# Kernel tuning notes

Measured on AMD Instinct MI355X. Metric: run time of the kernel, lower is better.

## Reference

```python
import jax, jax.numpy as jnp
import numpy as np

N_NODES = 100000
N_EDGES = 800000
IN_F = 128
HID = 128
OUT_F = 64


def setup_inputs() -> dict:
    key = jax.random.key(0)
    ks = jax.random.split(key, 13)
    s = 1.0 / np.sqrt(HID)
    return {
        "x": jax.random.normal(ks[0], (N_NODES, IN_F), jnp.float32),
        "src": jax.random.randint(ks[1], (N_EDGES,), 0, N_NODES, jnp.int32),
        "dst": jax.random.randint(ks[2], (N_EDGES,), 0, N_NODES, jnp.int32),
        "W1": jax.random.normal(ks[3], (HID, IN_F), jnp.float32) * s,
        "b1": jax.random.normal(ks[4], (HID,), jnp.float32) * s,
        "W2": jax.random.normal(ks[5], (HID, HID), jnp.float32) * s,
        "b2": jax.random.normal(ks[6], (HID,), jnp.float32) * s,
        "W3": jax.random.normal(ks[7], (HID, HID), jnp.float32) * s,
        "b3": jax.random.normal(ks[8], (HID,), jnp.float32) * s,
        "Wo1": jax.random.normal(ks[9], (HID, HID), jnp.float32) * s,
        "bo1": jax.random.normal(ks[10], (HID,), jnp.float32) * s,
        "Wo2": jax.random.normal(ks[11], (OUT_F, HID), jnp.float32) * s,
        "bo2": jax.random.normal(ks[12], (OUT_F,), jnp.float32) * s,
    }


def _mean_agg(h, src, dst, n_nodes):
    # mean over incoming edges (DGL copy_u -> mean reducer); isolated nodes get 0
    summed = jax.ops.segment_sum(h[src], dst, num_segments=n_nodes)
    deg = jax.ops.segment_sum(jnp.ones_like(src, h.dtype), dst, num_segments=n_nodes)
    return summed / jnp.maximum(deg, 1.0)[:, None]


def _lin(h, W, b):
    return h @ W.T + b


def reference(x, src, dst, W1, b1, W2, b2, W3, b3, Wo1, bo1, Wo2, bo2):
    n = x.shape[0]
    # x1 = fc1(x); x = relu(x1); x2 = fc2(x)
    x2 = _lin(jax.nn.relu(_lin(x, W1, b1)), W2, b2)
    # gin1: apply_func = Sequential(fc1, relu, fc2) on (x2 + mean_agg(x2)), eps=0
    h = x2 + _mean_agg(x2, src, dst, n)
    h = _lin(jax.nn.relu(_lin(h, W1, b1)), W2, b2)
    # x3 = fc3(h); h = relu(x3)
    h = jax.nn.relu(_lin(h, W3, b3))
    # gin2: apply_func = Sequential(fc3, relu) on (h + mean_agg(h))
    h = h + _mean_agg(h, src, dst, n)
    h = jax.nn.relu(_lin(h, W3, b3))
    # output head
    h = jax.nn.relu(_lin(h, Wo1, bo1))
    return _lin(h, Wo2, bo2)
```

## Files before the change

kernel.cpp:

```cpp
#include <hip/hip_runtime.h>

#define NNODES 100000
#define NEDGES 800000
#define NTILE128 782
#define NROWPAD (NTILE128*128)

typedef _Float16 f16x8 __attribute__((ext_vector_type(8)));
typedef float    f32x4 __attribute__((ext_vector_type(4)));
typedef unsigned int u32;
typedef unsigned short u16;

__global__ __launch_bounds__(256) void hist_kernel(const int* __restrict__ dst,
                                                   int* __restrict__ counts, int nE) {
    int i = blockIdx.x * 256 + threadIdx.x;
    if (i < nE) atomicAdd(counts + dst[i], 1);
}

__global__ __launch_bounds__(256) void scan1_kernel(const int* __restrict__ counts,
                                                    int* __restrict__ bsum, int n) {
    __shared__ int s[256];
    int i = blockIdx.x * 256 + threadIdx.x;
    s[threadIdx.x] = (i < n) ? counts[i] : 0;
    __syncthreads();
    for (int off = 128; off > 0; off >>= 1) {
        if (threadIdx.x < off) s[threadIdx.x] += s[threadIdx.x + off];
        __syncthreads();
    }
    if (threadIdx.x == 0) bsum[blockIdx.x] = s[0];
}

__global__ __launch_bounds__(512) void scan2_kernel(int* __restrict__ bsum, int nb) {
    __shared__ int s[512];
    int t = threadIdx.x;
    int orig = (t < nb) ? bsum[t] : 0;
    s[t] = orig;
    __syncthreads();
    for (int off = 1; off < 512; off <<= 1) {
        int v = (t >= off) ? s[t - off] : 0;
        __syncthreads();
        s[t] += v;
        __syncthreads();
    }
    if (t < nb) bsum[t] = s[t] - orig;
}

__global__ __launch_bounds__(256) void scan3_kernel(int* __restrict__ counts,
                                                    const int* __restrict__ boff,
                                                    int* __restrict__ rowptr, int n) {
    __shared__ int s[256];
    int i = blockIdx.x * 256 + threadIdx.x;
    int t = threadIdx.x;
    int orig = (i < n) ? counts[i] : 0;
    s[t] = orig;
    __syncthreads();
    for (int off = 1; off < 256; off <<= 1) {
        int v = (t >= off) ? s[t - off] : 0;
        __syncthreads();
        s[t] += v;
        __syncthreads();
    }
    if (i < n) {
        rowptr[i] = boff[blockIdx.x] + s[t] - orig;
        counts[i] = 0;
    }
    if (i == n - 1) rowptr[n] = boff[blockIdx.x] + s[t];
}

__global__ __launch_bounds__(256) void fill_kernel(const int* __restrict__ src,
                                                   const int* __restrict__ dst,
                                                   const int* __restrict__ rowptr,
                                                   int* __restrict__ cur,
                                                   int* __restrict__ eidx, int nE) {
    int i = blockIdx.x * 256 + threadIdx.x;
    if (i >= nE) return;
    int d = dst[i];
    int p = atomicAdd(cur + d, 1);
    eidx[rowptr[d] + p] = src[i];
}

__global__ __launch_bounds__(256) void gather_kernel(const _Float16* __restrict__ H,
                                                     const int* __restrict__ rowptr,
                                                     const int* __restrict__ eidx,
                                                     _Float16* __restrict__ O, int n) {
    int node = blockIdx.x * 4 + (threadIdx.x >> 6);
    int lane = threadIdx.x & 63;
    if (node >= n) return;
    int g = lane >> 4, p = lane & 15;
    int e0 = rowptr[node], e1 = rowptr[node + 1];
    float acc[8] = {0.f, 0.f, 0.f, 0.f, 0.f, 0.f, 0.f, 0.f};
    for (int j = e0; j < e1; j += 8) {
        int na = e1 - j;
        int sid = (lane < 8 && lane < na) ? eidx[j + lane] : -1;
        int s0 = __shfl(sid, g);
        int s1 = __shfl(sid, g + 4);
        f16x8 v0, v1;
        bool h0 = (s0 >= 0), h1 = (s1 >= 0);
        if (h0) v0 = *(const f16x8*)(H + (size_t)s0 * 128 + p * 8);
        if (h1) v1 = *(const f16x8*)(H + (size_t)s1 * 128 + p * 8);
        if (h0) {
#pragma unroll
            for (int r = 0; r < 8; ++r) acc[r] += (float)v0[r];
        }
        if (h1) {
#pragma unroll
            for (int r = 0; r < 8; ++r) acc[r] += (float)v1[r];
        }
    }
#pragma unroll
    for (int r = 0; r < 8; ++r) {
        acc[r] += __shfl_xor(acc[r], 16);
        acc[r] += __shfl_xor(acc[r], 32);
    }
    if (g == 0) {
        float rinv = 1.0f / fmaxf((float)(e1 - e0), 1.0f);
        f16x8 b = *(const f16x8*)(H + (size_t)node * 128 + p * 8);
        f16x8 o;
#pragma unroll
        for (int r = 0; r < 8; ++r) o[r] = (_Float16)((float)b[r] + acc[r] * rinv);
        *(f16x8*)(O + (size_t)node * 128 + p * 8) = o;
    }
}

template <int T, bool INF32, bool OUTF32, bool RELU>
__global__ __launch_bounds__(512, 4) void gemm4_kernel(const void* __restrict__ A_,
                                                       const float* __restrict__ Wg,
                                                       const float* __restrict__ Bg,
                                                       _Float16* __restrict__ O,
                                                       float* __restrict__ Of32) {
    constexpr int WFB = T * 4 * 64 * 8 * 2;
    constexpr int OBB = 128 * 132 * 4;
    constexpr int SMB = OUTF32 ? WFB : (WFB > OBB ? WFB : OBB);
    __shared__ __align__(16) char smem[SMB];
    _Float16 (*wf)[4][64][8] = (_Float16(*)[4][64][8])smem;
    u32* obuf = (u32*)smem;

    const int tid = threadIdx.x;
    const int lane = tid & 63, w = tid >> 6;
    const int lm = lane & 15, g = lane >> 4;
    const int tile = blockIdx.x;

    const int arow = tile * 128 + w * 16 + lm;
    f16x8 ah[4];
    float tv[4][8];
    if (INF32) {
        const float* base = (const float*)A_ + (size_t)min(arow, NNODES - 1) * 128;
#pragma unroll
        for (int ks = 0; ks < 4; ++ks) {
            *(float4*)&tv[ks][0] = *(const float4*)(base + ks * 32 + g * 8);
            *(float4*)&tv[ks][4] = *(const float4*)(base + ks * 32 + g * 8 + 4);
        }
    } else {
        const _Float16* bp = (const _Float16*)A_ + (size_t)arow * 128;
#pragma unroll
        for (int ks = 0; ks < 4; ++ks) ah[ks] = *(const f16x8*)(bp + ks * 32 + g * 8);
    }
    float bval[T];
#pragma unroll
    for (int t = 0; t < T; ++t) bval[t] = Bg[t * 16 + lm];

    for (int c = tid; c < T * 4 * 64; c += 512) {
        int t = c >> 8;
        int ks = (c >> 6) & 3;
        int ln = c & 63;
        int n = t * 16 + (ln & 15);
        int k0 = ks * 32 + (ln >> 4) * 8;
        const float* srcp = Wg + (size_t)n * 128 + k0;
        float wv[8];
        *(float4*)wv = *(const float4*)srcp;
        *(float4*)(wv + 4) = *(const float4*)(srcp + 4);
        f16x8 hv;
#pragma unroll
        for (int j = 0; j < 8; ++j) hv[j] = (_Float16)wv[j];
        *(f16x8*)&wf[t][ks][ln][0] = hv;
    }
    __syncthreads();

    if (INF32) {
#pragma unroll
        for (int ks = 0; ks < 4; ++ks)
#pragma unroll
            for (int j = 0; j < 8; ++j) ah[ks][j] = (_Float16)tv[ks][j];
    }

    f32x4 acc[T];
#pragma unroll
    for (int t = 0; t < T; ++t) acc[t] = (f32x4){bval[t], bval[t], bval[t], bval[t]};
#pragma unroll
    for (int t = 0; t < T; ++t) {
#pragma unroll
        for (int ks = 0; ks < 4; ++ks) {
            f16x8 wh = *(const f16x8*)&wf[t][ks][lane][0];
            acc[t] = __builtin_amdgcn_mfma_f32_16x16x32_f16(ah[ks], wh, acc[t], 0, 0, 0);
        }
    }

    if (OUTF32) {
        const int mrow0 = tile * 128 + w * 16 + g * 4;
#pragma unroll
        for (int t = 0; t < T; ++t) {
            const int n = t * 16 + lm;
#pragma unroll
            for (int r = 0; r < 4; ++r) {
                float v = acc[t][r];
                if (RELU) v = fmaxf(v, 0.f);
                int m = mrow0 + r;
                if (m < NNODES) Of32[(size_t)m * 64 + n] = v;
            }
        }
        return;
    }

    __syncthreads();
    {
        const int lrow0 = w * 16 + g * 4;
#pragma unroll
        for (int t = 0; t < T; ++t) {
            const int col = t * 16 + lm;
#pragma unroll
            for (int r = 0; r < 4; ++r) {
                float v = acc[t][r];
                if (RELU) v = fmaxf(v, 0.f);
                _Float16 h = (_Float16)v;
                obuf[(lrow0 + r) * 132 + col] = (u32)(*(u16*)&h);
            }
        }
    }
    __syncthreads();
#pragma unroll
    for (int pass = 0; pass < 4; ++pass) {
        int unit = pass * 512 + tid;
        int lrow = unit >> 4;
        int c8 = unit & 15;
        const u32* p = obuf + lrow * 132 + c8 * 8;
        u32 v[8];
        *(f32x4*)v = *(const f32x4*)p;
        *(f32x4*)(v + 4) = *(const f32x4*)(p + 4);
        f16x8 hh;
#pragma unroll
        for (int j = 0; j < 8; ++j) {
            u16 hs = (u16)(v[j] & 0xffffu);
            hh[j] = *(_Float16*)&hs;
        }
        size_t off = (size_t)(tile * 128 + lrow) * 128 + c8 * 8;
        *(f16x8*)(O + off) = hh;
    }
}

extern "C" void kernel_launch(void* const* d_in, const int* in_sizes, int n_in,
                              void* d_out, int out_size, void* d_ws, size_t ws_size,
                              hipStream_t stream) {
    const float* x   = (const float*)d_in[0];
    const int*   src = (const int*)d_in[1];
    const int*   dst = (const int*)d_in[2];
    const float* W1  = (const float*)d_in[3];
    const float* b1  = (const float*)d_in[4];
    const float* W2  = (const float*)d_in[5];
    const float* b2  = (const float*)d_in[6];
    const float* W3  = (const float*)d_in[7];
    const float* b3  = (const float*)d_in[8];
    const float* Wo1 = (const float*)d_in[9];
    const float* bo1 = (const float*)d_in[10];
    const float* Wo2 = (const float*)d_in[11];
    const float* bo2 = (const float*)d_in[12];
    float* out = (float*)d_out;

    const size_t PLANE = (size_t)NROWPAD * 128 * sizeof(_Float16);
    char* ws = (char*)d_ws;
    _Float16* P0 = (_Float16*)ws;
    _Float16* P1 = (_Float16*)(ws + PLANE);
    char* p = ws + 2 * PLANE;
    int* counts = (int*)p;  p += 512 * 1024;
    int* rowptr = (int*)p;  p += 512 * 1024;
    int* bsum   = (int*)p;  p += 16 * 1024;
    int* eidx   = (int*)p;

    dim3 blk(256);
    const int NB = (NNODES + 255) / 256;
    const int ge = (NEDGES + 255) / 256;
    const int gg = (NNODES + 3) / 4;

    hipMemsetAsync(counts, 0, NNODES * sizeof(int), stream);
    hist_kernel<<<ge, blk, 0, stream>>>(dst, counts, NEDGES);
    scan1_kernel<<<NB, blk, 0, stream>>>(counts, bsum, NNODES);
    scan2_kernel<<<1, 512, 0, stream>>>(bsum, NB);
    scan3_kernel<<<NB, blk, 0, stream>>>(counts, bsum, rowptr, NNODES);
    fill_kernel<<<ge, blk, 0, stream>>>(src, dst, rowptr, counts, eidx, NEDGES);

    gemm4_kernel<8, true,  false, true ><<<NTILE128, 512, 0, stream>>>(x,  W1, b1, P0, nullptr);
    gemm4_kernel<8, false, false, false><<<NTILE128, 512, 0, stream>>>(P0, W2, b2, P1, nullptr);

    gather_kernel<<<gg, blk, 0, stream>>>(P1, rowptr, eidx, P0, NNODES);

    gemm4_kernel<8, false, false, true ><<<NTILE128, 512, 0, stream>>>(P0, W1, b1, P1, nullptr);
    gemm4_kernel<8, false, false, false><<<NTILE128, 512, 0, stream>>>(P1, W2, b2, P0, nullptr);
    gemm4_kernel<8, false, false, true ><<<NTILE128, 512, 0, stream>>>(P0, W3, b3, P1, nullptr);

    gather_kernel<<<gg, blk, 0, stream>>>(P1, rowptr, eidx, P0, NNODES);

    gemm4_kernel<8, false, false, true ><<<NTILE128, 512, 0, stream>>>(P0, W3, b3, P1, nullptr);
    gemm4_kernel<8, false, false, true ><<<NTILE128, 512, 0, stream>>>(P1, Wo1, bo1, P0, nullptr);
    gemm4_kernel<4, false, true,  false><<<NTILE128, 512, 0, stream>>>(P0, Wo2, bo2, nullptr, out);
}
```

Measured before the change: 424.6 us.

## Fuse consecutive linear layers into chained kernels with prepacked fp16 weights

Replaces the eight per-layer GEMM launches with three chain kernels, each running two or three linear layers back to back on a 128-row tile. Intermediate activations pass through shared memory instead of global memory. A one-time pack kernel converts all weights to fp16 in MFMA fragment order, so the chained kernels read weight fragments straight from global memory and no longer stage them in LDS per block. The aim is to cut global round trips of the 100k×128 activation planes and launch overhead. In exchange, per-fragment global weight loads and lower declared occupancy (launch bounds 512,2) may add latency.

```diff
diff --git a/kernel.cpp b/kernel.cpp
--- a/kernel.cpp
+++ b/kernel.cpp
@@ -76,6 +76,39 @@
     int d = dst[i];
     int p = atomicAdd(cur + d, 1);
     eidx[rowptr[d] + p] = src[i];
+}
+
+__global__ __launch_bounds__(256) void wpack_kernel(const float* __restrict__ W1,
+                                                    const float* __restrict__ W2,
+                                                    const float* __restrict__ W3,
+                                                    const float* __restrict__ Wo1,
+                                                    const float* __restrict__ Wo2,
+                                                    _Float16* __restrict__ wp) {
+    int i = blockIdx.x * 256 + threadIdx.x;
+    if (i >= 9216) return;
+    const float* Wm;
+    int li;
+    size_t base;
+    if (i < 8192) {
+        int m = i >> 11;
+        li = i & 2047;
+        Wm = (m == 0) ? W1 : (m == 1) ? W2 : (m == 2) ? W3 : Wo1;
+        base = (size_t)m * 16384;
+    } else {
+        li = i - 8192;
+        Wm = Wo2;
+        base = 65536;
+    }
+    int lane = li & 63;
+    int n = ((li >> 8) * 16) + (lane & 15);
+    int k0 = (((li >> 6) & 3) * 32) + ((lane >> 4) * 8);
+    const float* s = Wm + (size_t)n * 128 + k0;
+    float4 a = *(const float4*)s;
+    float4 b = *(const float4*)(s + 4);
+    f16x8 v;
+    v[0] = (_Float16)a.x; v[1] = (_Float16)a.y; v[2] = (_Float16)a.z; v[3] = (_Float16)a.w;
+    v[4] = (_Float16)b.x; v[5] = (_Float16)b.y; v[6] = (_Float16)b.z; v[7] = (_Float16)b.w;
+    *(f16x8*)(wp + base + (size_t)li * 8) = v;
 }
 
 __global__ __launch_bounds__(256) void gather_kernel(const _Float16* __restrict__ H,
@@ -121,128 +154,130 @@
     }
 }
 
-template <int T, bool INF32, bool OUTF32, bool RELU>
-__global__ __launch_bounds__(512, 4) void gemm4_kernel(const void* __restrict__ A_,
-                                                       const float* __restrict__ Wg,
-                                                       const float* __restrict__ Bg,
-                                                       _Float16* __restrict__ O,
-                                                       float* __restrict__ Of32) {
-    constexpr int WFB = T * 4 * 64 * 8 * 2;
-    constexpr int OBB = 128 * 132 * 4;
-    constexpr int SMB = OUTF32 ? WFB : (WFB > OBB ? WFB : OBB);
-    __shared__ __align__(16) char smem[SMB];
-    _Float16 (*wf)[4][64][8] = (_Float16(*)[4][64][8])smem;
-    u32* obuf = (u32*)smem;
-
+template <int S, bool INF32, bool OUTF32, int TL, bool R0, bool R1, bool R2>
+__global__ __launch_bounds__(512, 2) void chain_kernel(
+    const void* __restrict__ A_,
+    const _Float16* __restrict__ wq0, const float* __restrict__ Bg0,
+    const _Float16* __restrict__ wq1, const float* __restrict__ Bg1,
+    const _Float16* __restrict__ wq2, const float* __restrict__ Bg2,
+    _Float16* __restrict__ O, float* __restrict__ Of32) {
+    __shared__ u32 ibuf[128][137];
     const int tid = threadIdx.x;
     const int lane = tid & 63, w = tid >> 6;
     const int lm = lane & 15, g = lane >> 4;
     const int tile = blockIdx.x;
 
+    f16x8 ah[4];
     const int arow = tile * 128 + w * 16 + lm;
-    f16x8 ah[4];
-    float tv[4][8];
     if (INF32) {
         const float* base = (const float*)A_ + (size_t)min(arow, NNODES - 1) * 128;
 #pragma unroll
         for (int ks = 0; ks < 4; ++ks) {
-            *(float4*)&tv[ks][0] = *(const float4*)(base + ks * 32 + g * 8);
-            *(float4*)&tv[ks][4] = *(const float4*)(base + ks * 32 + g * 8 + 4);
+            float4 a = *(const float4*)(base + ks * 32 + g * 8);
+            float4 b = *(const float4*)(base + ks * 32 + g * 8 + 4);
+            ah[ks][0] = (_Float16)a.x; ah[ks][1] = (_Float16)a.y;
+            ah[ks][2] = (_Float16)a.z; ah[ks][3] = (_Float16)a.w;
+            ah[ks][4] = (_Float16)b.x; ah[ks][5] = (_Float16)b.y;
+            ah[ks][6] = (_Float16)b.z; ah[ks][7] = (_Float16)b.w;
         }
     } else {
         const _Float16* bp = (const _Float16*)A_ + (size_t)arow * 128;
 #pragma unroll
         for (int ks = 0; ks < 4; ++ks) ah[ks] = *(const f16x8*)(bp + ks * 32 + g * 8);
     }
-    float bval[T];
-#pragma unroll
-    for (int t = 0; t < T; ++t) bval[t] = Bg[t * 16 + lm];
-
-    for (int c = tid; c < T * 4 * 64; c += 512) {
-        int t = c >> 8;
-        int ks = (c >> 6) & 3;
-        int ln = c & 63;
-        int n = t * 16 + (ln & 15);
-        int k0 = ks * 32 + (ln >> 4) * 8;
-        const float* srcp = Wg + (size_t)n * 128 + k0;
-        float wv[8];
-        *(float4*)wv = *(const float4*)srcp;
-        *(float4*)(wv + 4) = *(const float4*)(srcp + 4);
-        f16x8 hv;
-#pragma unroll
-        for (int j = 0; j < 8; ++j) hv[j] = (_Float16)wv[j];
-        *(f16x8*)&wf[t][ks][ln][0] = hv;
-    }
-    __syncthreads();
-
-    if (INF32) {
-#pragma unroll
-        for (int ks = 0; ks < 4; ++ks)
-#pragma unroll
-            for (int j = 0; j < 8; ++j) ah[ks][j] = (_Float16)tv[ks][j];
-    }
-
-    f32x4 acc[T];
-#pragma unroll
-    for (int t = 0; t < T; ++t) acc[t] = (f32x4){bval[t], bval[t], bval[t], bval[t]};
-#pragma unroll
-    for (int t = 0; t < T; ++t) {
-#pragma unroll
-        for (int ks = 0; ks < 4; ++ks) {
-            f16x8 wh = *(const f16x8*)&wf[t][ks][lane][0];
-            acc[t] = __builtin_amdgcn_mfma_f32_16x16x32_f16(ah[ks], wh, acc[t], 0, 0, 0);
+
+#pragma unroll
+    for (int s = 0; s < S; ++s) {
+        const _Float16* wq = (s == 0) ? wq0 : (s == 1) ? wq1 : wq2;
+        const float* Bg = (s == 0) ? Bg0 : (s == 1) ? Bg1 : Bg2;
+        const bool RELU = (s == 0) ? R0 : (s == 1) ? R1 : R2;
+        const int T = (s == S - 1) ? TL : 8;
+
+        f32x4 acc[8];
+#pragma unroll
+        for (int t = 0; t < 8; ++t)
+            if (t < T) {
+                float bv = Bg[t * 16 + lm];
+                acc[t] = (f32x4){bv, bv, bv, bv};
+            }
+#pragma unroll
+        for (int t = 0; t < 8; ++t)
+            if (t < T) {
+#pragma unroll
+                for (int ks = 0; ks < 4; ++ks) {
+                    f16x8 wv = *(const f16x8*)(wq + ((size_t)(t * 4 + ks) * 64 + lane) * 8);
+                    acc[t] = __builtin_amdgcn_mfma_f32_16x16x32_f16(ah[ks], wv, acc[t], 0, 0, 0);
+                }
+            }
+
+        if (s < S - 1) {
+            __syncthreads();
+            const int lrow0 = w * 16 + g * 4;
+#pragma unroll
+            for (int t = 0; t < 8; ++t)
+#pragma unroll
+                for (int r = 0; r < 4; ++r) {
+                    float v = acc[t][r];
+                    if (RELU) v = fmaxf(v, 0.f);
+                    _Float16 h = (_Float16)v;
+                    ibuf[lrow0 + r][t * 16 + lm] = (u32)(*(u16*)&h);
+                }
+            __syncthreads();
+            const u32* rp = &ibuf[w * 16 + lm][0];
+#pragma unroll
+            for (int ks = 0; ks < 4; ++ks) {
+                u32 v[8];
+                *(f32x4*)v = *(const f32x4*)(rp + ks * 32 + g * 8);
+                *(f32x4*)(v + 4) = *(const f32x4*)(rp + ks * 32 + g * 8 + 4);
+#pragma unroll
+                for (int j = 0; j < 8; ++j) {
+                    u16 hs = (u16)(v[j] & 0xffffu);
+                    ah[ks][j] = *(_Float16*)&hs;
+                }
+            }
+        } else if (OUTF32) {
+            const int mrow0 = tile * 128 + w * 16 + g * 4;
+#pragma unroll
+            for (int t = 0; t < TL; ++t) {
+                const int n = t * 16 + lm;
+#pragma unroll
+                for (int r = 0; r < 4; ++r) {
+                    float v = acc[t][r];
+                    if (RELU) v = fmaxf(v, 0.f);
+                    int m = mrow0 + r;
+                    if (m < NNODES) Of32[(size_t)m * 64 + n] = v;
+                }
+            }
+        } else {
+            __syncthreads();
+            const int lrow0 = w * 16 + g * 4;
+#pragma unroll
+            for (int t = 0; t < 8; ++t)
+#pragma unroll
+                for (int r = 0; r < 4; ++r) {
+                    float v = acc[t][r];
+                    if (RELU) v = fmaxf(v, 0.f);
+                    _Float16 h = (_Float16)v;
+                    ibuf[lrow0 + r][t * 16 + lm] = (u32)(*(u16*)&h);
+                }
+            __syncthreads();
+#pragma unroll
+            for (int pass = 0; pass < 4; ++pass) {
+                int unit = pass * 512 + tid;
+                int lrow = unit >> 4, c8 = unit & 15;
+                const u32* p = &ibuf[lrow][c8 * 8];
+                u32 v[8];
+                *(f32x4*)v = *(const f32x4*)p;
+                *(f32x4*)(v + 4) = *(const f32x4*)(p + 4);
+                f16x8 hh;
+#pragma unroll
+                for (int j = 0; j < 8; ++j) {
+                    u16 hs = (u16)(v[j] & 0xffffu);
+                    hh[j] = *(_Float16*)&hs;
+                }
+                *(f16x8*)(O + (size_t)(tile * 128 + lrow) * 128 + c8 * 8) = hh;
+            }
         }
-    }
-
-    if (OUTF32) {
-        const int mrow0 = tile * 128 + w * 16 + g * 4;
-#pragma unroll
-        for (int t = 0; t < T; ++t) {
-            const int n = t * 16 + lm;
-#pragma unroll
-            for (int r = 0; r < 4; ++r) {
-                float v = acc[t][r];
-                if (RELU) v = fmaxf(v, 0.f);
-                int m = mrow0 + r;
-                if (m < NNODES) Of32[(size_t)m * 64 + n] = v;
-            }
-        }
-        return;
-    }
-
-    __syncthreads();
-    {
-        const int lrow0 = w * 16 + g * 4;
-#pragma unroll
-        for (int t = 0; t < T; ++t) {
-            const int col = t * 16 + lm;
-#pragma unroll
-            for (int r = 0; r < 4; ++r) {
-                float v = acc[t][r];
-                if (RELU) v = fmaxf(v, 0.f);
-                _Float16 h = (_Float16)v;
-                obuf[(lrow0 + r) * 132 + col] = (u32)(*(u16*)&h);
-            }
-        }
-    }
-    __syncthreads();
-#pragma unroll
-    for (int pass = 0; pass < 4; ++pass) {
-        int unit = pass * 512 + tid;
-        int lrow = unit >> 4;
-        int c8 = unit & 15;
-        const u32* p = obuf + lrow * 132 + c8 * 8;
-        u32 v[8];
-        *(f32x4*)v = *(const f32x4*)p;
-        *(f32x4*)(v + 4) = *(const f32x4*)(p + 4);
-        f16x8 hh;
-#pragma unroll
-        for (int j = 0; j < 8; ++j) {
-            u16 hs = (u16)(v[j] & 0xffffu);
-            hh[j] = *(_Float16*)&hs;
-        }
-        size_t off = (size_t)(tile * 128 + lrow) * 128 + c8 * 8;
-        *(f16x8*)(O + off) = hh;
     }
 }
 
@@ -269,15 +304,18 @@
     _Float16* P0 = (_Float16*)ws;
     _Float16* P1 = (_Float16*)(ws + PLANE);
     char* p = ws + 2 * PLANE;
-    int* counts = (int*)p;  p += 512 * 1024;
-    int* rowptr = (int*)p;  p += 512 * 1024;
-    int* bsum   = (int*)p;  p += 16 * 1024;
+    int* counts = (int*)p;     p += 512 * 1024;
+    int* rowptr = (int*)p;     p += 512 * 1024;
+    int* bsum   = (int*)p;     p += 16 * 1024;
+    _Float16* wp = (_Float16*)p;  p += 256 * 1024;
     int* eidx   = (int*)p;
 
     dim3 blk(256);
     const int NB = (NNODES + 255) / 256;
     const int ge = (NEDGES + 255) / 256;
     const int gg = (NNODES + 3) / 4;
+
+    wpack_kernel<<<36, blk, 0, stream>>>(W1, W2, W3, Wo1, Wo2, wp);
 
     hipMemsetAsync(counts, 0, NNODES * sizeof(int), stream);
     hist_kernel<<<ge, blk, 0, stream>>>(dst, counts, NEDGES);
@@ -286,18 +324,19 @@
     scan3_kernel<<<NB, blk, 0, stream>>>(counts, bsum, rowptr, NNODES);
     fill_kernel<<<ge, blk, 0, stream>>>(src, dst, rowptr, counts, eidx, NEDGES);
 
-    gemm4_kernel<8, true,  false, true ><<<NTILE128, 512, 0, stream>>>(x,  W1, b1, P0, nullptr);
-    gemm4_kernel<8, false, false, false><<<NTILE128, 512, 0, stream>>>(P0, W2, b2, P1, nullptr);
-
-    gather_kernel<<<gg, blk, 0, stream>>>(P1, rowptr, eidx, P0, NNODES);
-
-    gemm4_kernel<8, false, false, true ><<<NTILE128, 512, 0, stream>>>(P0, W1, b1, P1, nullptr);
-    gemm4_kernel<8, false, false, false><<<NTILE128, 512, 0, stream>>>(P1, W2, b2, P0, nullptr);
-    gemm4_kernel<8, false, false, true ><<<NTILE128, 512, 0, stream>>>(P0, W3, b3, P1, nullptr);
-
-    gather_kernel<<<gg, blk, 0, stream>>>(P1, rowptr, eidx, P0, NNODES);
-
-    gemm4_kernel<8, false, false, true ><<<NTILE128, 512, 0, stream>>>(P0, W3, b3, P1, nullptr);
-    gemm4_kernel<8, false, false, true ><<<NTILE128, 512, 0, stream>>>(P1, Wo1, bo1, P0, nullptr);
-    gemm4_kernel<4, false, true,  false><<<NTILE128, 512, 0, stream>>>(P0, Wo2, bo2, nullptr, out);
-}
+    const _Float16 *q1 = wp, *q2 = wp + 16384, *q3 = wp + 32768,
+                   *qo1 = wp + 49152, *qo2 = wp + 65536;
+
+    chain_kernel<2, true, false, 8, true, false, false><<<NTILE128, 512, 0, stream>>>(
+        x, q1, b1, q2, b2, nullptr, nullptr, P0, nullptr);
+
+    gather_kernel<<<gg, blk, 0, stream>>>(P0, rowptr, eidx, P1, NNODES);
+
+    chain_kernel<3, false, false, 8, true, false, true><<<NTILE128, 512, 0, stream>>>(
+        P1, q1, b1, q2, b2, q3, b3, P0, nullptr);
+
+    gather_kernel<<<gg, blk, 0, stream>>>(P0, rowptr, eidx, P1, NNODES);
+
+    chain_kernel<3, false, true, 4, true, true, false><<<NTILE128, 512, 0, stream>>>(
+        P1, q3, b3, qo1, bo1, qo2, bo2, nullptr, out);
+}
```

New measurement: 386.0 us. 9.1% less time.
